# Performance work log

Hardware: AMD Instinct MI355X
Metric: run time of the kernel (lower is better)

## Reference

```python
import jax, jax.numpy as jnp
import numpy as np

D_MODEL = 1024
N_HEAD = 16
D_HEAD = D_MODEL // N_HEAD


def setup_inputs() -> dict:
    key = jax.random.key(0)
    k_x, k_qkv, k_proj = jax.random.split(key, 3)
    B, T = 2, 2048
    x = jax.random.normal(k_x, (B, T, D_MODEL), dtype=jnp.float32)
    # torch Linear weight [out, in]; y = x @ W.T. Scale ~ kaiming-uniform-ish.
    s = 1.0 / np.sqrt(D_MODEL)
    W_qkv = jax.random.uniform(k_qkv, (3 * D_MODEL, D_MODEL), dtype=jnp.float32, minval=-s, maxval=s)
    W_proj = jax.random.uniform(k_proj, (D_MODEL, D_MODEL), dtype=jnp.float32, minval=-s, maxval=s)
    return {"x": x, "W_qkv": W_qkv, "W_proj": W_proj}


def reference(x, W_qkv, W_proj):
    B, T, C = x.shape
    qkv = jnp.einsum('btc,oc->bto', x, W_qkv)  # [B,T,3C]
    q, k, v = jnp.split(qkv, 3, axis=-1)
    # [B,T,C] -> [B,H,T,Dh]
    def heads(t):
        return t.reshape(B, T, N_HEAD, D_HEAD).transpose(0, 2, 1, 3)
    q, k, v = heads(q), heads(k), heads(v)
    scale = 1.0 / np.sqrt(D_HEAD)
    scores = jnp.einsum('bhqd,bhkd->bhqk', q, k) * scale  # [B,H,T,T]
    causal = jnp.tril(jnp.ones((T, T), dtype=bool))
    scores = jnp.where(causal, scores, jnp.finfo(scores.dtype).min)
    attn = jax.nn.softmax(scores, axis=-1)
    y = jnp.einsum('bhqk,bhkd->bhqd', attn, v)  # [B,H,T,Dh]
    y = y.transpose(0, 2, 1, 3).reshape(B, T, C)
    return jnp.einsum('btc,oc->bto', y, W_proj)
```

## Files before the change

kernel.cpp:

```cpp
#include <hip/hip_runtime.h>

typedef unsigned short u16;
typedef float f32x4 __attribute__((ext_vector_type(4)));
typedef __bf16 bf16x8 __attribute__((ext_vector_type(8)));
typedef unsigned int u32x4 __attribute__((ext_vector_type(4)));
typedef u16 u16x4 __attribute__((ext_vector_type(4)));
typedef u16 u16x8 __attribute__((ext_vector_type(8)));

static __device__ __forceinline__ u16 f2bf(float f) {
  union { __bf16 h; u16 u; } c;
  c.h = (__bf16)f;
  return c.u;
}

static __device__ __forceinline__ void gload_lds16(const void* g, void* l) {
  __builtin_amdgcn_global_load_lds(
      (const __attribute__((address_space(1))) unsigned int*)g,
      (__attribute__((address_space(3))) unsigned int*)l, 16, 0, 0);
}

__global__ __launch_bounds__(256) void cvt3_f32_bf16(const float* __restrict__ a,
                                                     const float* __restrict__ bb,
                                                     const float* __restrict__ cc,
                                                     u16* __restrict__ out,
                                                     int n1, int n2, int n3) {
  int i = blockIdx.x * 256 + threadIdx.x;
  const float* src;
  int j = i;
  if (i < n1) { src = a; }
  else if (i < n1 + n2) { src = bb; j = i - n1; }
  else { src = cc; j = i - n1 - n2; if (j >= n3) return; }
  f32x4 v = *((const f32x4*)src + j);
  u16x4 o;
  o[0] = f2bf(v[0]); o[1] = f2bf(v[1]); o[2] = f2bf(v[2]); o[3] = f2bf(v[3]);
  *((u16x4*)out + i) = o;
}

template<int OUT_BF16>
__global__ __launch_bounds__(256) void gemm_nt(const u16* __restrict__ A,
                                               const u16* __restrict__ B,
                                               void* __restrict__ Cp,
                                               int M, int N, int K, int gy) {
  __shared__ __align__(16) u16 lA[128 * 64];
  __shared__ __align__(16) u16 lB[128 * 64];
  const int tid = threadIdx.x;
  const int lane = tid & 63;
  const int wave = tid >> 6;
  const int wm = wave >> 1, wn = wave & 1;
  const int l15 = lane & 15, lg = lane >> 4;

  const int bid = blockIdx.x;
  const int xcd = bid & 7, s = bid >> 3;
  const int pnx = (N >> 7) >> 3;
  const int bm = (s % gy) * 128;
  const int bn = (xcd * pnx + s / gy) * 128;

  f32x4 acc[4][4];
#pragma unroll
  for (int i = 0; i < 4; ++i)
#pragma unroll
    for (int j = 0; j < 4; ++j) acc[i][j] = (f32x4){0.f, 0.f, 0.f, 0.f};

  const u16* Ag[4];
  const u16* Bg[4];
#pragma unroll
  for (int it = 0; it < 4; ++it) {
    const int ss = it * 256 + tid;
    const int row = ss >> 3, g = ss & 7;
    const int gsw = g ^ (row & 7);
    Ag[it] = A + (size_t)(bm + row) * K + gsw * 8;
    Bg[it] = B + (size_t)(bn + row) * K + gsw * 8;
  }

  for (int k0 = 0; k0 < K; k0 += 64) {
#pragma unroll
    for (int it = 0; it < 4; ++it) {
      gload_lds16(Ag[it] + k0, (u16*)lA + (size_t)(it * 256 + tid) * 8);
      gload_lds16(Bg[it] + k0, (u16*)lB + (size_t)(it * 256 + tid) * 8);
    }
    __syncthreads();
#pragma unroll
    for (int kk = 0; kk < 2; ++kk) {
      bf16x8 af[4], bfv[4];
#pragma unroll
      for (int mf = 0; mf < 4; ++mf) {
        const int row = wm * 64 + mf * 16 + l15;
        af[mf] = *(const bf16x8*)((const char*)lA + row * 128 +
                                  ((kk * 64 + lg * 16) ^ ((row & 7) << 4)));
      }
#pragma unroll
      for (int nf = 0; nf < 4; ++nf) {
        const int row = wn * 64 + nf * 16 + l15;
        bfv[nf] = *(const bf16x8*)((const char*)lB + row * 128 +
                                   ((kk * 64 + lg * 16) ^ ((row & 7) << 4)));
      }
#pragma unroll
      for (int mf = 0; mf < 4; ++mf)
#pragma unroll
        for (int nf = 0; nf < 4; ++nf)
          acc[mf][nf] = __builtin_amdgcn_mfma_f32_16x16x32_bf16(af[mf], bfv[nf], acc[mf][nf], 0, 0, 0);
    }
    __syncthreads();
  }

#pragma unroll
  for (int mf = 0; mf < 4; ++mf) {
#pragma unroll
    for (int r = 0; r < 4; ++r) {
      const int row = bm + wm * 64 + mf * 16 + lg * 4 + r;
#pragma unroll
      for (int nf = 0; nf < 4; ++nf) {
        const int col = bn + wn * 64 + nf * 16 + l15;
        const float v = acc[mf][nf][r];
        if (OUT_BF16) ((u16*)Cp)[(size_t)row * N + col] = f2bf(v);
        else          ((float*)Cp)[(size_t)row * N + col] = v;
      }
    }
  }
}

__global__ __launch_bounds__(256) void transpose_v(const u16* __restrict__ qkv,
                                                   u16* __restrict__ vt) {
  constexpr int T = 2048, C3 = 3072, D = 64;
  __shared__ u16 lt[64 * 65];
  const int t0 = blockIdx.x * 64;
  const int bh = blockIdx.y;
  const int b = bh >> 4, h = bh & 15;
  const int tid = threadIdx.x;
#pragma unroll
  for (int it = 0; it < 2; ++it) {
    const int c = tid + it * 256;
    const int tr = c >> 3, d0 = (c & 7) * 8;
    u32x4 v = *(const u32x4*)&qkv[((size_t)b * T + t0 + tr) * C3 + 2048 + h * D + d0];
    const u16* pv = (const u16*)&v;
#pragma unroll
    for (int e = 0; e < 8; ++e) lt[tr * 65 + d0 + e] = pv[e];
  }
  __syncthreads();
#pragma unroll
  for (int it = 0; it < 2; ++it) {
    const int c = tid + it * 256;
    const int d = c >> 3, toff = (c & 7) * 8;
    u16x8 tmp;
#pragma unroll
    for (int e = 0; e < 8; ++e) tmp[e] = lt[(toff + e) * 65 + d];
    *(u16x8*)&vt[((size_t)bh * D + d) * T + t0 + toff] = tmp;
  }
}

__global__ __launch_bounds__(256) void attn_fwd(const u16* __restrict__ qkv,
                                                const u16* __restrict__ vt,
                                                u16* __restrict__ y) {
  constexpr int T = 2048, C = 1024, C3 = 3072, D = 64, NQ = 32;
  __shared__ __align__(16) u16 lK[2][64 * 64];
  __shared__ __align__(16) u16 lV[2][64 * 64];
  __shared__ __align__(16) u16 lP[4 * 16 * 64];
  const int tid = threadIdx.x, lane = tid & 63, w = tid >> 6;
  const int l15 = lane & 15, lg = lane >> 4;

  const int bid = blockIdx.x;
  const int xcd = bid & 7, slot = bid >> 3;
  const int bh = xcd * 4 + (slot >> 4);
  const int pi = slot & 15;
  const int b = bh >> 4, h = bh & 15;

  const int r0 = tid >> 3, off0 = (tid & 7) * 8;
  const int r1 = (tid + 256) >> 3, off1 = off0;
  const int sb0 = (off0 * 2) ^ ((r0 & 7) << 4);
  const int sb1 = (off1 * 2) ^ ((r1 & 7) << 4);
  const u16* Kbase = qkv + (size_t)b * T * C3 + C + h * D;
  const u16* Vbase = vt + (size_t)bh * D * T;

  const float qscale = 0.125f * 1.44269504088896f;

#pragma unroll 1
  for (int qi = 0; qi < 2; ++qi) {
    const int qt = (qi == 0) ? pi : (NQ - 1 - pi);
    const int q0 = qt * 64;

    const size_t qoff = ((size_t)b * T + q0 + w * 16 + l15) * C3 + h * D;
    const bf16x8 aq0 = *(const bf16x8*)&qkv[qoff + lg * 8];
    const bf16x8 aq1 = *(const bf16x8*)&qkv[qoff + 32 + lg * 8];

    float m = -1.0e30f, l = 0.f;
    f32x4 o_acc[4];
#pragma unroll
    for (int nf = 0; nf < 4; ++nf) o_acc[nf] = (f32x4){0.f, 0.f, 0.f, 0.f};

    u32x4 rk0 = *(const u32x4*)(Kbase + (size_t)r0 * C3 + off0);
    u32x4 rk1 = *(const u32x4*)(Kbase + (size_t)r1 * C3 + off1);
    u32x4 rv0 = *(const u32x4*)(Vbase + (size_t)r0 * T + off0);
    u32x4 rv1 = *(const u32x4*)(Vbase + (size_t)r1 * T + off1);
    __syncthreads();
    *(u32x4*)&lK[0][(r0 * 128 + sb0) >> 1] = rk0;
    *(u32x4*)&lK[0][(r1 * 128 + sb1) >> 1] = rk1;
    *(u32x4*)&lV[0][(r0 * 128 + sb0) >> 1] = rv0;
    *(u32x4*)&lV[0][(r1 * 128 + sb1) >> 1] = rv1;
    if (qt > 0) {
      rk0 = *(const u32x4*)(Kbase + (size_t)(64 + r0) * C3 + off0);
      rk1 = *(const u32x4*)(Kbase + (size_t)(64 + r1) * C3 + off1);
      rv0 = *(const u32x4*)(Vbase + (size_t)r0 * T + 64 + off0);
      rv1 = *(const u32x4*)(Vbase + (size_t)r1 * T + 64 + off1);
    }

    for (int kt = 0; kt <= qt; ++kt) {
      const int cur = kt & 1;
      __syncthreads();
      if (kt < qt) {
        *(u32x4*)&lK[cur ^ 1][(r0 * 128 + sb0) >> 1] = rk0;
        *(u32x4*)&lK[cur ^ 1][(r1 * 128 + sb1) >> 1] = rk1;
        *(u32x4*)&lV[cur ^ 1][(r0 * 128 + sb0) >> 1] = rv0;
        *(u32x4*)&lV[cur ^ 1][(r1 * 128 + sb1) >> 1] = rv1;
        if (kt + 1 < qt) {
          const int kn = (kt + 2) * 64;
          rk0 = *(const u32x4*)(Kbase + (size_t)(kn + r0) * C3 + off0);
          rk1 = *(const u32x4*)(Kbase + (size_t)(kn + r1) * C3 + off1);
          rv0 = *(const u32x4*)(Vbase + (size_t)r0 * T + kn + off0);
          rv1 = *(const u32x4*)(Vbase + (size_t)r1 * T + kn + off1);
        }
      }
      const u16* Kc = lK[cur];
      const u16* Vc = lV[cur];

      f32x4 s[4];
#pragma unroll
      for (int nf = 0; nf < 4; ++nf) s[nf] = (f32x4){0.f, 0.f, 0.f, 0.f};
      __builtin_amdgcn_s_setprio(1);
#pragma unroll
      for (int nf = 0; nf < 4; ++nf) {
        const int row = nf * 16 + l15;
        const int x = (row & 7) << 4;
        bf16x8 bk0 = *(const bf16x8*)&Kc[(row * 128 + ((lg * 16) ^ x)) >> 1];
        bf16x8 bk1 = *(const bf16x8*)&Kc[(row * 128 + ((64 + lg * 16) ^ x)) >> 1];
        s[nf] = __builtin_amdgcn_mfma_f32_16x16x32_bf16(bk0, aq0, s[nf], 0, 0, 0);
        s[nf] = __builtin_amdgcn_mfma_f32_16x16x32_bf16(bk1, aq1, s[nf], 0, 0, 0);
      }
      __builtin_amdgcn_s_setprio(0);

#pragma unroll
      for (int nf = 0; nf < 4; ++nf) {
#pragma unroll
        for (int r = 0; r < 4; ++r) {
          float v = s[nf][r] * qscale;
          if (kt == qt) {
            if (nf * 16 + lg * 4 + r > w * 16 + l15) v = -1.0e30f;
          }
          s[nf][r] = v;
        }
      }

      float t0a = fmaxf(fmaxf(s[0][0], s[0][1]), fmaxf(s[0][2], s[0][3]));
      float t1a = fmaxf(fmaxf(s[1][0], s[1][1]), fmaxf(s[1][2], s[1][3]));
      float t2a = fmaxf(fmaxf(s[2][0], s[2][1]), fmaxf(s[2][2], s[2][3]));
      float t3a = fmaxf(fmaxf(s[3][0], s[3][1]), fmaxf(s[3][2], s[3][3]));
      float pmax = fmaxf(fmaxf(t0a, t1a), fmaxf(t2a, t3a));
      pmax = fmaxf(pmax, __shfl_xor(pmax, 16));
      pmax = fmaxf(pmax, __shfl_xor(pmax, 32));

      if (!__all(pmax <= m)) {
        const float mnew = fmaxf(m, pmax);
        const float fct = __builtin_amdgcn_exp2f(m - mnew);
        m = mnew;
        l *= fct;
#pragma unroll
        for (int r = 0; r < 4; ++r) {
          const float fr = __shfl(fct, lg * 4 + r);
#pragma unroll
          for (int nf = 0; nf < 4; ++nf) o_acc[nf][r] *= fr;
        }
      }

      float p[4][4];
#pragma unroll
      for (int nf = 0; nf < 4; ++nf)
#pragma unroll
        for (int r = 0; r < 4; ++r) p[nf][r] = __builtin_amdgcn_exp2f(s[nf][r] - m);
      float s0a = (p[0][0] + p[0][1]) + (p[0][2] + p[0][3]);
      float s1a = (p[1][0] + p[1][1]) + (p[1][2] + p[1][3]);
      float s2a = (p[2][0] + p[2][1]) + (p[2][2] + p[2][3]);
      float s3a = (p[3][0] + p[3][1]) + (p[3][2] + p[3][3]);
      float psum = (s0a + s1a) + (s2a + s3a);
      psum += __shfl_xor(psum, 16);
      psum += __shfl_xor(psum, 32);
      l += psum;

#pragma unroll
      for (int nf = 0; nf < 4; ++nf) {
        u16x4 pk;
        pk[0] = f2bf(p[nf][0]); pk[1] = f2bf(p[nf][1]);
        pk[2] = f2bf(p[nf][2]); pk[3] = f2bf(p[nf][3]);
        *(u16x4*)&lP[(w * 2048 + l15 * 128 + ((nf * 32 + lg * 8) ^ ((l15 & 7) << 4))) >> 1] = pk;
      }

      __builtin_amdgcn_s_setprio(1);
#pragma unroll
      for (int sj = 0; sj < 2; ++sj) {
        bf16x8 ap = *(const bf16x8*)&lP[(w * 2048 + l15 * 128 + ((sj * 64 + lg * 16) ^ ((l15 & 7) << 4))) >> 1];
#pragma unroll
        for (int nf = 0; nf < 4; ++nf) {
          const int d = nf * 16 + l15;
          bf16x8 bv = *(const bf16x8*)&Vc[(d * 128 + ((sj * 64 + lg * 16) ^ ((d & 7) << 4))) >> 1];
          o_acc[nf] = __builtin_amdgcn_mfma_f32_16x16x32_bf16(ap, bv, o_acc[nf], 0, 0, 0);
        }
      }
      __builtin_amdgcn_s_setprio(0);
    }

#pragma unroll
    for (int r = 0; r < 4; ++r) {
      const float li = __builtin_amdgcn_rcpf(__shfl(l, lg * 4 + r));
      const int row = q0 + w * 16 + lg * 4 + r;
#pragma unroll
      for (int nf = 0; nf < 4; ++nf) {
        const int col = h * D + nf * 16 + l15;
        y[((size_t)b * T + row) * C + col] = f2bf(o_acc[nf][r] * li);
      }
    }
  }
}

extern "C" void kernel_launch(void* const* d_in, const int* in_sizes, int n_in,
                              void* d_out, int out_size, void* d_ws, size_t ws_size,
                              hipStream_t stream) {
  const float* x = (const float*)d_in[0];
  const float* Wqkv = (const float*)d_in[1];
  const float* Wproj = (const float*)d_in[2];
  float* out = (float*)d_out;

  constexpr int B = 2, T = 2048, C = 1024, C3 = 3072, H = 16, D = 64;
  constexpr int M = B * T;

  u16* xb = (u16*)d_ws;
  u16* wqkvb = xb + (size_t)M * C;
  u16* wprojb = wqkvb + (size_t)C3 * C;
  u16* qkvb = wprojb + (size_t)C * C;
  u16* vtb = qkvb + (size_t)M * C3;
  u16* yb = vtb + (size_t)M * C;

  constexpr int n1 = (M * C) / 4, n2 = (C3 * C) / 4, n3 = (C * C) / 4;
  cvt3_f32_bf16<<<dim3((n1 + n2 + n3 + 255) / 256), 256, 0, stream>>>(
      x, Wqkv, Wproj, xb, n1, n2, n3);

  gemm_nt<1><<<dim3((C3 / 128) * (M / 128)), 256, 0, stream>>>(xb, wqkvb, qkvb, M, C3, C, M / 128);
  transpose_v<<<dim3(T / 64, B * H), 256, 0, stream>>>(qkvb, vtb);
  attn_fwd<<<dim3(512), 256, 0, stream>>>(qkvb, vtb, yb);
  gemm_nt<0><<<dim3((C / 128) * (M / 128)), 256, 0, stream>>>(yb, wprojb, out, M, C, C, M / 128);
}
```

Before: 115.4 us.

## Fuse V transpose into QKV GEMM epilogue and widen attention key tiles

The QKV GEMM epilogue now writes the V columns directly into the transposed per-head layout, which removes the separate transpose_v kernel launch and its extra read/write pass. The attention kernel also processes 128-key tiles instead of 64, with LDS buffers for K, V and P doubled and the swizzles adjusted. This halves the number of loop iterations and barriers per query tile. The cost is more registers and LDS per block, which may lower occupancy, plus some wasted masked work on the final diagonal tile.

```diff
diff --git a/kernel.cpp b/kernel.cpp
--- a/kernel.cpp
+++ b/kernel.cpp
@@ -36,10 +36,11 @@
   *((u16x4*)out + i) = o;
 }
 
-template<int OUT_BF16>
+template<int OUT_BF16, int FUSE_VT>
 __global__ __launch_bounds__(256) void gemm_nt(const u16* __restrict__ A,
                                                const u16* __restrict__ B,
                                                void* __restrict__ Cp,
+                                               u16* __restrict__ vt,
                                                int M, int N, int K, int gy) {
   __shared__ __align__(16) u16 lA[128 * 64];
   __shared__ __align__(16) u16 lB[128 * 64];
@@ -103,58 +104,46 @@
     __syncthreads();
   }
 
-#pragma unroll
-  for (int mf = 0; mf < 4; ++mf) {
-#pragma unroll
-    for (int r = 0; r < 4; ++r) {
-      const int row = bm + wm * 64 + mf * 16 + lg * 4 + r;
+  if (FUSE_VT && bn >= 2048) {
+#pragma unroll
+    for (int mf = 0; mf < 4; ++mf) {
+      const int row0 = bm + wm * 64 + mf * 16 + lg * 4;
+      const int b = row0 >> 11, t0 = row0 & 2047;
 #pragma unroll
       for (int nf = 0; nf < 4; ++nf) {
-        const int col = bn + wn * 64 + nf * 16 + l15;
-        const float v = acc[mf][nf][r];
-        if (OUT_BF16) ((u16*)Cp)[(size_t)row * N + col] = f2bf(v);
-        else          ((float*)Cp)[(size_t)row * N + col] = v;
-      }
-    }
-  }
-}
-
-__global__ __launch_bounds__(256) void transpose_v(const u16* __restrict__ qkv,
-                                                   u16* __restrict__ vt) {
-  constexpr int T = 2048, C3 = 3072, D = 64;
-  __shared__ u16 lt[64 * 65];
-  const int t0 = blockIdx.x * 64;
-  const int bh = blockIdx.y;
-  const int b = bh >> 4, h = bh & 15;
-  const int tid = threadIdx.x;
-#pragma unroll
-  for (int it = 0; it < 2; ++it) {
-    const int c = tid + it * 256;
-    const int tr = c >> 3, d0 = (c & 7) * 8;
-    u32x4 v = *(const u32x4*)&qkv[((size_t)b * T + t0 + tr) * C3 + 2048 + h * D + d0];
-    const u16* pv = (const u16*)&v;
-#pragma unroll
-    for (int e = 0; e < 8; ++e) lt[tr * 65 + d0 + e] = pv[e];
-  }
-  __syncthreads();
-#pragma unroll
-  for (int it = 0; it < 2; ++it) {
-    const int c = tid + it * 256;
-    const int d = c >> 3, toff = (c & 7) * 8;
-    u16x8 tmp;
-#pragma unroll
-    for (int e = 0; e < 8; ++e) tmp[e] = lt[(toff + e) * 65 + d];
-    *(u16x8*)&vt[((size_t)bh * D + d) * T + t0 + toff] = tmp;
+        const int colv = bn - 2048 + wn * 64 + nf * 16 + l15;
+        const int h = colv >> 6, d = colv & 63;
+        u16x4 pk;
+        pk[0] = f2bf(acc[mf][nf][0]); pk[1] = f2bf(acc[mf][nf][1]);
+        pk[2] = f2bf(acc[mf][nf][2]); pk[3] = f2bf(acc[mf][nf][3]);
+        *(u16x4*)&vt[((size_t)((b * 16 + h) * 64 + d)) * 2048 + t0] = pk;
+      }
+    }
+  } else {
+#pragma unroll
+    for (int mf = 0; mf < 4; ++mf) {
+#pragma unroll
+      for (int r = 0; r < 4; ++r) {
+        const int row = bm + wm * 64 + mf * 16 + lg * 4 + r;
+#pragma unroll
+        for (int nf = 0; nf < 4; ++nf) {
+          const int col = bn + wn * 64 + nf * 16 + l15;
+          const float v = acc[mf][nf][r];
+          if (OUT_BF16) ((u16*)Cp)[(size_t)row * N + col] = f2bf(v);
+          else          ((float*)Cp)[(size_t)row * N + col] = v;
+        }
+      }
+    }
   }
 }
 
 __global__ __launch_bounds__(256) void attn_fwd(const u16* __restrict__ qkv,
                                                 const u16* __restrict__ vt,
                                                 u16* __restrict__ y) {
-  constexpr int T = 2048, C = 1024, C3 = 3072, D = 64, NQ = 32;
-  __shared__ __align__(16) u16 lK[2][64 * 64];
-  __shared__ __align__(16) u16 lV[2][64 * 64];
-  __shared__ __align__(16) u16 lP[4 * 16 * 64];
+  constexpr int T = 2048, C = 1024, C3 = 3072, D = 64, NQ = 32, KB = 128;
+  __shared__ __align__(16) u16 lK[2][KB * 64];
+  __shared__ __align__(16) u16 lV[2][64 * KB];
+  __shared__ __align__(16) u16 lP[4 * 16 * KB];
   const int tid = threadIdx.x, lane = tid & 63, w = tid >> 6;
   const int l15 = lane & 15, lg = lane >> 4;
 
@@ -164,12 +153,18 @@
   const int pi = slot & 15;
   const int b = bh >> 4, h = bh & 15;
 
-  const int r0 = tid >> 3, off0 = (tid & 7) * 8;
-  const int r1 = (tid + 256) >> 3, off1 = off0;
-  const int sb0 = (off0 * 2) ^ ((r0 & 7) << 4);
-  const int sb1 = (off1 * 2) ^ ((r1 & 7) << 4);
+  int kr[4], ko[4], ksb[4], vd[4], vo[4], vsb[4];
+#pragma unroll
+  for (int c = 0; c < 4; ++c) {
+    const int fl = c * 256 + tid;
+    kr[c] = fl >> 3; ko[c] = (fl & 7) * 8;
+    ksb[c] = kr[c] * 128 + ((ko[c] * 2) ^ ((kr[c] & 7) << 4));
+    vd[c] = fl >> 4; vo[c] = (fl & 15) * 8;
+    vsb[c] = vd[c] * 256 + ((vo[c] * 2) ^ ((vd[c] & 15) << 4));
+  }
   const u16* Kbase = qkv + (size_t)b * T * C3 + C + h * D;
   const u16* Vbase = vt + (size_t)bh * D * T;
+  char* lPb = (char*)lP + w * 4096;
 
   const float qscale = 0.125f * 1.44269504088896f;
 
@@ -177,8 +172,10 @@
   for (int qi = 0; qi < 2; ++qi) {
     const int qt = (qi == 0) ? pi : (NQ - 1 - pi);
     const int q0 = qt * 64;
-
-    const size_t qoff = ((size_t)b * T + q0 + w * 16 + l15) * C3 + h * D;
+    const int nkt = (qt + 2) >> 1;
+    const int qrow = q0 + w * 16 + l15;
+
+    const size_t qoff = ((size_t)b * T + qrow) * C3 + h * D;
     const bf16x8 aq0 = *(const bf16x8*)&qkv[qoff + lg * 8];
     const bf16x8 aq1 = *(const bf16x8*)&qkv[qoff + 32 + lg * 8];
 
@@ -187,73 +184,85 @@
 #pragma unroll
     for (int nf = 0; nf < 4; ++nf) o_acc[nf] = (f32x4){0.f, 0.f, 0.f, 0.f};
 
-    u32x4 rk0 = *(const u32x4*)(Kbase + (size_t)r0 * C3 + off0);
-    u32x4 rk1 = *(const u32x4*)(Kbase + (size_t)r1 * C3 + off1);
-    u32x4 rv0 = *(const u32x4*)(Vbase + (size_t)r0 * T + off0);
-    u32x4 rv1 = *(const u32x4*)(Vbase + (size_t)r1 * T + off1);
+    u32x4 rk[4], rv[4];
+#pragma unroll
+    for (int c = 0; c < 4; ++c) {
+      rk[c] = *(const u32x4*)(Kbase + (size_t)kr[c] * C3 + ko[c]);
+      rv[c] = *(const u32x4*)(Vbase + (size_t)vd[c] * T + vo[c]);
+    }
     __syncthreads();
-    *(u32x4*)&lK[0][(r0 * 128 + sb0) >> 1] = rk0;
-    *(u32x4*)&lK[0][(r1 * 128 + sb1) >> 1] = rk1;
-    *(u32x4*)&lV[0][(r0 * 128 + sb0) >> 1] = rv0;
-    *(u32x4*)&lV[0][(r1 * 128 + sb1) >> 1] = rv1;
-    if (qt > 0) {
-      rk0 = *(const u32x4*)(Kbase + (size_t)(64 + r0) * C3 + off0);
-      rk1 = *(const u32x4*)(Kbase + (size_t)(64 + r1) * C3 + off1);
-      rv0 = *(const u32x4*)(Vbase + (size_t)r0 * T + 64 + off0);
-      rv1 = *(const u32x4*)(Vbase + (size_t)r1 * T + 64 + off1);
-    }
-
-    for (int kt = 0; kt <= qt; ++kt) {
+#pragma unroll
+    for (int c = 0; c < 4; ++c) {
+      *(u32x4*)((char*)lK[0] + ksb[c]) = rk[c];
+      *(u32x4*)((char*)lV[0] + vsb[c]) = rv[c];
+    }
+    if (nkt > 1) {
+#pragma unroll
+      for (int c = 0; c < 4; ++c) {
+        rk[c] = *(const u32x4*)(Kbase + (size_t)(KB + kr[c]) * C3 + ko[c]);
+        rv[c] = *(const u32x4*)(Vbase + (size_t)vd[c] * T + KB + vo[c]);
+      }
+    }
+
+    for (int kt = 0; kt < nkt; ++kt) {
       const int cur = kt & 1;
       __syncthreads();
-      if (kt < qt) {
-        *(u32x4*)&lK[cur ^ 1][(r0 * 128 + sb0) >> 1] = rk0;
-        *(u32x4*)&lK[cur ^ 1][(r1 * 128 + sb1) >> 1] = rk1;
-        *(u32x4*)&lV[cur ^ 1][(r0 * 128 + sb0) >> 1] = rv0;
-        *(u32x4*)&lV[cur ^ 1][(r1 * 128 + sb1) >> 1] = rv1;
-        if (kt + 1 < qt) {
-          const int kn = (kt + 2) * 64;
-          rk0 = *(const u32x4*)(Kbase + (size_t)(kn + r0) * C3 + off0);
-          rk1 = *(const u32x4*)(Kbase + (size_t)(kn + r1) * C3 + off1);
-          rv0 = *(const u32x4*)(Vbase + (size_t)r0 * T + kn + off0);
-          rv1 = *(const u32x4*)(Vbase + (size_t)r1 * T + kn + off1);
-        }
-      }
-      const u16* Kc = lK[cur];
-      const u16* Vc = lV[cur];
-
-      f32x4 s[4];
-#pragma unroll
-      for (int nf = 0; nf < 4; ++nf) s[nf] = (f32x4){0.f, 0.f, 0.f, 0.f};
+      if (kt < nkt - 1) {
+#pragma unroll
+        for (int c = 0; c < 4; ++c) {
+          *(u32x4*)((char*)lK[cur ^ 1] + ksb[c]) = rk[c];
+          *(u32x4*)((char*)lV[cur ^ 1] + vsb[c]) = rv[c];
+        }
+        if (kt + 1 < nkt - 1) {
+          const int kn = (kt + 2) * KB;
+#pragma unroll
+          for (int c = 0; c < 4; ++c) {
+            rk[c] = *(const u32x4*)(Kbase + (size_t)(kn + kr[c]) * C3 + ko[c]);
+            rv[c] = *(const u32x4*)(Vbase + (size_t)vd[c] * T + kn + vo[c]);
+          }
+        }
+      }
+      const char* Kc = (const char*)lK[cur];
+      const char* Vc = (const char*)lV[cur];
+
+      f32x4 s[8];
+#pragma unroll
+      for (int nf = 0; nf < 8; ++nf) s[nf] = (f32x4){0.f, 0.f, 0.f, 0.f};
       __builtin_amdgcn_s_setprio(1);
 #pragma unroll
-      for (int nf = 0; nf < 4; ++nf) {
+      for (int nf = 0; nf < 8; ++nf) {
         const int row = nf * 16 + l15;
         const int x = (row & 7) << 4;
-        bf16x8 bk0 = *(const bf16x8*)&Kc[(row * 128 + ((lg * 16) ^ x)) >> 1];
-        bf16x8 bk1 = *(const bf16x8*)&Kc[(row * 128 + ((64 + lg * 16) ^ x)) >> 1];
+        bf16x8 bk0 = *(const bf16x8*)(Kc + row * 128 + ((lg * 16) ^ x));
+        bf16x8 bk1 = *(const bf16x8*)(Kc + row * 128 + ((64 + lg * 16) ^ x));
         s[nf] = __builtin_amdgcn_mfma_f32_16x16x32_bf16(bk0, aq0, s[nf], 0, 0, 0);
         s[nf] = __builtin_amdgcn_mfma_f32_16x16x32_bf16(bk1, aq1, s[nf], 0, 0, 0);
       }
       __builtin_amdgcn_s_setprio(0);
 
-#pragma unroll
-      for (int nf = 0; nf < 4; ++nf) {
-#pragma unroll
-        for (int r = 0; r < 4; ++r) {
-          float v = s[nf][r] * qscale;
-          if (kt == qt) {
-            if (nf * 16 + lg * 4 + r > w * 16 + l15) v = -1.0e30f;
+      if (kt == nkt - 1) {
+        const int qrel = qrow - kt * KB;
+#pragma unroll
+        for (int nf = 0; nf < 8; ++nf)
+#pragma unroll
+          for (int r = 0; r < 4; ++r) {
+            float v = s[nf][r] * qscale;
+            if (nf * 16 + lg * 4 + r > qrel) v = -1.0e30f;
+            s[nf][r] = v;
           }
-          s[nf][r] = v;
-        }
-      }
-
-      float t0a = fmaxf(fmaxf(s[0][0], s[0][1]), fmaxf(s[0][2], s[0][3]));
-      float t1a = fmaxf(fmaxf(s[1][0], s[1][1]), fmaxf(s[1][2], s[1][3]));
-      float t2a = fmaxf(fmaxf(s[2][0], s[2][1]), fmaxf(s[2][2], s[2][3]));
-      float t3a = fmaxf(fmaxf(s[3][0], s[3][1]), fmaxf(s[3][2], s[3][3]));
-      float pmax = fmaxf(fmaxf(t0a, t1a), fmaxf(t2a, t3a));
+      } else {
+#pragma unroll
+        for (int nf = 0; nf < 8; ++nf)
+#pragma unroll
+          for (int r = 0; r < 4; ++r) s[nf][r] *= qscale;
+      }
+
+      float q4[8];
+#pragma unroll
+      for (int nf = 0; nf < 8; ++nf)
+        q4[nf] = fmaxf(fmaxf(s[nf][0], s[nf][1]), fmaxf(s[nf][2], s[nf][3]));
+      float pmax = fmaxf(fmaxf(fmaxf(q4[0], q4[1]), fmaxf(q4[2], q4[3])),
+                         fmaxf(fmaxf(q4[4], q4[5]), fmaxf(q4[6], q4[7])));
       pmax = fmaxf(pmax, __shfl_xor(pmax, 16));
       pmax = fmaxf(pmax, __shfl_xor(pmax, 32));
 
@@ -270,36 +279,35 @@
         }
       }
 
-      float p[4][4];
-#pragma unroll
-      for (int nf = 0; nf < 4; ++nf)
-#pragma unroll
-        for (int r = 0; r < 4; ++r) p[nf][r] = __builtin_amdgcn_exp2f(s[nf][r] - m);
-      float s0a = (p[0][0] + p[0][1]) + (p[0][2] + p[0][3]);
-      float s1a = (p[1][0] + p[1][1]) + (p[1][2] + p[1][3]);
-      float s2a = (p[2][0] + p[2][1]) + (p[2][2] + p[2][3]);
-      float s3a = (p[3][0] + p[3][1]) + (p[3][2] + p[3][3]);
-      float psum = (s0a + s1a) + (s2a + s3a);
+#pragma unroll
+      for (int nf = 0; nf < 8; ++nf)
+#pragma unroll
+        for (int r = 0; r < 4; ++r) s[nf][r] = __builtin_amdgcn_exp2f(s[nf][r] - m);
+      float a4[8];
+#pragma unroll
+      for (int nf = 0; nf < 8; ++nf)
+        a4[nf] = (s[nf][0] + s[nf][1]) + (s[nf][2] + s[nf][3]);
+      float psum = ((a4[0] + a4[1]) + (a4[2] + a4[3])) + ((a4[4] + a4[5]) + (a4[6] + a4[7]));
       psum += __shfl_xor(psum, 16);
       psum += __shfl_xor(psum, 32);
       l += psum;
 
 #pragma unroll
-      for (int nf = 0; nf < 4; ++nf) {
+      for (int nf = 0; nf < 8; ++nf) {
         u16x4 pk;
-        pk[0] = f2bf(p[nf][0]); pk[1] = f2bf(p[nf][1]);
-        pk[2] = f2bf(p[nf][2]); pk[3] = f2bf(p[nf][3]);
-        *(u16x4*)&lP[(w * 2048 + l15 * 128 + ((nf * 32 + lg * 8) ^ ((l15 & 7) << 4))) >> 1] = pk;
+        pk[0] = f2bf(s[nf][0]); pk[1] = f2bf(s[nf][1]);
+        pk[2] = f2bf(s[nf][2]); pk[3] = f2bf(s[nf][3]);
+        *(u16x4*)(lPb + l15 * 256 + ((nf * 32 + lg * 8) ^ (l15 << 4))) = pk;
       }
 
       __builtin_amdgcn_s_setprio(1);
 #pragma unroll
-      for (int sj = 0; sj < 2; ++sj) {
-        bf16x8 ap = *(const bf16x8*)&lP[(w * 2048 + l15 * 128 + ((sj * 64 + lg * 16) ^ ((l15 & 7) << 4))) >> 1];
+      for (int sj = 0; sj < 4; ++sj) {
+        bf16x8 ap = *(const bf16x8*)(lPb + l15 * 256 + ((sj * 64 + lg * 16) ^ (l15 << 4)));
 #pragma unroll
         for (int nf = 0; nf < 4; ++nf) {
           const int d = nf * 16 + l15;
-          bf16x8 bv = *(const bf16x8*)&Vc[(d * 128 + ((sj * 64 + lg * 16) ^ ((d & 7) << 4))) >> 1];
+          bf16x8 bv = *(const bf16x8*)(Vc + d * 256 + ((sj * 64 + lg * 16) ^ ((d & 15) << 4)));
           o_acc[nf] = __builtin_amdgcn_mfma_f32_16x16x32_bf16(ap, bv, o_acc[nf], 0, 0, 0);
         }
       }
@@ -341,8 +349,9 @@
   cvt3_f32_bf16<<<dim3((n1 + n2 + n3 + 255) / 256), 256, 0, stream>>>(
       x, Wqkv, Wproj, xb, n1, n2, n3);
 
-  gemm_nt<1><<<dim3((C3 / 128) * (M / 128)), 256, 0, stream>>>(xb, wqkvb, qkvb, M, C3, C, M / 128);
-  transpose_v<<<dim3(T / 64, B * H), 256, 0, stream>>>(qkvb, vtb);
+  gemm_nt<1, 1><<<dim3((C3 / 128) * (M / 128)), 256, 0, stream>>>(
+      xb, wqkvb, qkvb, vtb, M, C3, C, M / 128);
   attn_fwd<<<dim3(512), 256, 0, stream>>>(qkvb, vtb, yb);
-  gemm_nt<0><<<dim3((C / 128) * (M / 128)), 256, 0, stream>>>(yb, wprojb, out, M, C, C, M / 128);
-}
+  gemm_nt<0, 0><<<dim3((C / 128) * (M / 128)), 256, 0, stream>>>(
+      yb, wprojb, out, nullptr, M, C, C, M / 128);
+}
```

New measurement: 129.4 us. +12.2%, slower.

## Split attention KV range across two blocks and fuse V transpose into QKV GEMM

Applied to the files above, without the earlier changes.

Attention now launches twice as many blocks, each handling half of the causal KV range for a query tile. Each block writes a partial output plus its running max and sum, and a new merge kernel combines the two halves. Separately, the QKV GEMM epilogue writes the V columns directly in transposed layout, which removes the standalone transpose kernel. The aim is more parallelism and better occupancy in attention and one fewer launch, at the cost of an extra merge kernel, partial-output round trips through memory, and a second bf16 rounding of the partial outputs.

```diff
diff --git a/kernel.cpp b/kernel.cpp
--- a/kernel.cpp
+++ b/kernel.cpp
@@ -11,6 +11,11 @@
   union { __bf16 h; u16 u; } c;
   c.h = (__bf16)f;
   return c.u;
+}
+static __device__ __forceinline__ float bf2f(u16 u) {
+  union { unsigned u; float f; } c;
+  c.u = ((unsigned)u) << 16;
+  return c.f;
 }
 
 static __device__ __forceinline__ void gload_lds16(const void* g, void* l) {
@@ -36,10 +41,11 @@
   *((u16x4*)out + i) = o;
 }
 
-template<int OUT_BF16>
+template<int OUT_BF16, int FUSE_VT>
 __global__ __launch_bounds__(256) void gemm_nt(const u16* __restrict__ A,
                                                const u16* __restrict__ B,
                                                void* __restrict__ Cp,
+                                               u16* __restrict__ vt,
                                                int M, int N, int K, int gy) {
   __shared__ __align__(16) u16 lA[128 * 64];
   __shared__ __align__(16) u16 lB[128 * 64];
@@ -103,54 +109,43 @@
     __syncthreads();
   }
 
-#pragma unroll
-  for (int mf = 0; mf < 4; ++mf) {
-#pragma unroll
-    for (int r = 0; r < 4; ++r) {
-      const int row = bm + wm * 64 + mf * 16 + lg * 4 + r;
+  if (FUSE_VT && bn >= 2048) {
+#pragma unroll
+    for (int mf = 0; mf < 4; ++mf) {
+      const int row0 = bm + wm * 64 + mf * 16 + lg * 4;
+      const int b = row0 >> 11, t0 = row0 & 2047;
 #pragma unroll
       for (int nf = 0; nf < 4; ++nf) {
-        const int col = bn + wn * 64 + nf * 16 + l15;
-        const float v = acc[mf][nf][r];
-        if (OUT_BF16) ((u16*)Cp)[(size_t)row * N + col] = f2bf(v);
-        else          ((float*)Cp)[(size_t)row * N + col] = v;
-      }
-    }
-  }
-}
-
-__global__ __launch_bounds__(256) void transpose_v(const u16* __restrict__ qkv,
-                                                   u16* __restrict__ vt) {
-  constexpr int T = 2048, C3 = 3072, D = 64;
-  __shared__ u16 lt[64 * 65];
-  const int t0 = blockIdx.x * 64;
-  const int bh = blockIdx.y;
-  const int b = bh >> 4, h = bh & 15;
-  const int tid = threadIdx.x;
-#pragma unroll
-  for (int it = 0; it < 2; ++it) {
-    const int c = tid + it * 256;
-    const int tr = c >> 3, d0 = (c & 7) * 8;
-    u32x4 v = *(const u32x4*)&qkv[((size_t)b * T + t0 + tr) * C3 + 2048 + h * D + d0];
-    const u16* pv = (const u16*)&v;
-#pragma unroll
-    for (int e = 0; e < 8; ++e) lt[tr * 65 + d0 + e] = pv[e];
-  }
-  __syncthreads();
-#pragma unroll
-  for (int it = 0; it < 2; ++it) {
-    const int c = tid + it * 256;
-    const int d = c >> 3, toff = (c & 7) * 8;
-    u16x8 tmp;
-#pragma unroll
-    for (int e = 0; e < 8; ++e) tmp[e] = lt[(toff + e) * 65 + d];
-    *(u16x8*)&vt[((size_t)bh * D + d) * T + t0 + toff] = tmp;
+        const int colv = bn - 2048 + wn * 64 + nf * 16 + l15;
+        const int h = colv >> 6, d = colv & 63;
+        u16x4 pk;
+        pk[0] = f2bf(acc[mf][nf][0]); pk[1] = f2bf(acc[mf][nf][1]);
+        pk[2] = f2bf(acc[mf][nf][2]); pk[3] = f2bf(acc[mf][nf][3]);
+        *(u16x4*)&vt[((size_t)((b * 16 + h) * 64 + d)) * 2048 + t0] = pk;
+      }
+    }
+  } else {
+#pragma unroll
+    for (int mf = 0; mf < 4; ++mf) {
+#pragma unroll
+      for (int r = 0; r < 4; ++r) {
+        const int row = bm + wm * 64 + mf * 16 + lg * 4 + r;
+#pragma unroll
+        for (int nf = 0; nf < 4; ++nf) {
+          const int col = bn + wn * 64 + nf * 16 + l15;
+          const float v = acc[mf][nf][r];
+          if (OUT_BF16) ((u16*)Cp)[(size_t)row * N + col] = f2bf(v);
+          else          ((float*)Cp)[(size_t)row * N + col] = v;
+        }
+      }
+    }
   }
 }
 
 __global__ __launch_bounds__(256) void attn_fwd(const u16* __restrict__ qkv,
                                                 const u16* __restrict__ vt,
-                                                u16* __restrict__ y) {
+                                                u16* __restrict__ po,
+                                                float* __restrict__ mlf) {
   constexpr int T = 2048, C = 1024, C3 = 3072, D = 64, NQ = 32;
   __shared__ __align__(16) u16 lK[2][64 * 64];
   __shared__ __align__(16) u16 lV[2][64 * 64];
@@ -159,15 +154,16 @@
   const int l15 = lane & 15, lg = lane >> 4;
 
   const int bid = blockIdx.x;
-  const int xcd = bid & 7, slot = bid >> 3;
-  const int bh = xcd * 4 + (slot >> 4);
-  const int pi = slot & 15;
+  const int xcd = bid & 7, rest = bid >> 3;
+  const int bhl = rest >> 5, r5 = rest & 31;
+  const int pi = r5 >> 1, hf = r5 & 1;
+  const int bh = xcd * 4 + bhl;
   const int b = bh >> 4, h = bh & 15;
 
   const int r0 = tid >> 3, off0 = (tid & 7) * 8;
-  const int r1 = (tid + 256) >> 3, off1 = off0;
+  const int r1 = (tid + 256) >> 3;
   const int sb0 = (off0 * 2) ^ ((r0 & 7) << 4);
-  const int sb1 = (off1 * 2) ^ ((r1 & 7) << 4);
+  const int sb1 = (off0 * 2) ^ ((r1 & 7) << 4);
   const u16* Kbase = qkv + (size_t)b * T * C3 + C + h * D;
   const u16* Vbase = vt + (size_t)bh * D * T;
 
@@ -177,6 +173,10 @@
   for (int qi = 0; qi < 2; ++qi) {
     const int qt = (qi == 0) ? pi : (NQ - 1 - pi);
     const int q0 = qt * 64;
+    const int h0 = (qt + 2) >> 1;
+    const int kts = hf ? h0 : 0;
+    const int kte = hf ? (qt + 1) : h0;
+    const int nit = kte - kts;
 
     const size_t qoff = ((size_t)b * T + q0 + w * 16 + l15) * C3 + h * D;
     const bf16x8 aq0 = *(const bf16x8*)&qkv[qoff + lg * 8];
@@ -187,136 +187,171 @@
 #pragma unroll
     for (int nf = 0; nf < 4; ++nf) o_acc[nf] = (f32x4){0.f, 0.f, 0.f, 0.f};
 
-    u32x4 rk0 = *(const u32x4*)(Kbase + (size_t)r0 * C3 + off0);
-    u32x4 rk1 = *(const u32x4*)(Kbase + (size_t)r1 * C3 + off1);
-    u32x4 rv0 = *(const u32x4*)(Vbase + (size_t)r0 * T + off0);
-    u32x4 rv1 = *(const u32x4*)(Vbase + (size_t)r1 * T + off1);
-    __syncthreads();
-    *(u32x4*)&lK[0][(r0 * 128 + sb0) >> 1] = rk0;
-    *(u32x4*)&lK[0][(r1 * 128 + sb1) >> 1] = rk1;
-    *(u32x4*)&lV[0][(r0 * 128 + sb0) >> 1] = rv0;
-    *(u32x4*)&lV[0][(r1 * 128 + sb1) >> 1] = rv1;
-    if (qt > 0) {
-      rk0 = *(const u32x4*)(Kbase + (size_t)(64 + r0) * C3 + off0);
-      rk1 = *(const u32x4*)(Kbase + (size_t)(64 + r1) * C3 + off1);
-      rv0 = *(const u32x4*)(Vbase + (size_t)r0 * T + 64 + off0);
-      rv1 = *(const u32x4*)(Vbase + (size_t)r1 * T + 64 + off1);
-    }
-
-    for (int kt = 0; kt <= qt; ++kt) {
-      const int cur = kt & 1;
+    if (nit > 0) {
+      const int kb0 = kts * 64;
+      u32x4 rk0 = *(const u32x4*)(Kbase + (size_t)(kb0 + r0) * C3 + off0);
+      u32x4 rk1 = *(const u32x4*)(Kbase + (size_t)(kb0 + r1) * C3 + off0);
+      u32x4 rv0 = *(const u32x4*)(Vbase + (size_t)r0 * T + kb0 + off0);
+      u32x4 rv1 = *(const u32x4*)(Vbase + (size_t)r1 * T + kb0 + off0);
       __syncthreads();
-      if (kt < qt) {
-        *(u32x4*)&lK[cur ^ 1][(r0 * 128 + sb0) >> 1] = rk0;
-        *(u32x4*)&lK[cur ^ 1][(r1 * 128 + sb1) >> 1] = rk1;
-        *(u32x4*)&lV[cur ^ 1][(r0 * 128 + sb0) >> 1] = rv0;
-        *(u32x4*)&lV[cur ^ 1][(r1 * 128 + sb1) >> 1] = rv1;
-        if (kt + 1 < qt) {
-          const int kn = (kt + 2) * 64;
-          rk0 = *(const u32x4*)(Kbase + (size_t)(kn + r0) * C3 + off0);
-          rk1 = *(const u32x4*)(Kbase + (size_t)(kn + r1) * C3 + off1);
-          rv0 = *(const u32x4*)(Vbase + (size_t)r0 * T + kn + off0);
-          rv1 = *(const u32x4*)(Vbase + (size_t)r1 * T + kn + off1);
-        }
-      }
-      const u16* Kc = lK[cur];
-      const u16* Vc = lV[cur];
-
-      f32x4 s[4];
-#pragma unroll
-      for (int nf = 0; nf < 4; ++nf) s[nf] = (f32x4){0.f, 0.f, 0.f, 0.f};
-      __builtin_amdgcn_s_setprio(1);
-#pragma unroll
-      for (int nf = 0; nf < 4; ++nf) {
-        const int row = nf * 16 + l15;
-        const int x = (row & 7) << 4;
-        bf16x8 bk0 = *(const bf16x8*)&Kc[(row * 128 + ((lg * 16) ^ x)) >> 1];
-        bf16x8 bk1 = *(const bf16x8*)&Kc[(row * 128 + ((64 + lg * 16) ^ x)) >> 1];
-        s[nf] = __builtin_amdgcn_mfma_f32_16x16x32_bf16(bk0, aq0, s[nf], 0, 0, 0);
-        s[nf] = __builtin_amdgcn_mfma_f32_16x16x32_bf16(bk1, aq1, s[nf], 0, 0, 0);
-      }
-      __builtin_amdgcn_s_setprio(0);
-
-#pragma unroll
-      for (int nf = 0; nf < 4; ++nf) {
-#pragma unroll
-        for (int r = 0; r < 4; ++r) {
-          float v = s[nf][r] * qscale;
-          if (kt == qt) {
-            if (nf * 16 + lg * 4 + r > w * 16 + l15) v = -1.0e30f;
+      *(u32x4*)&lK[0][(r0 * 128 + sb0) >> 1] = rk0;
+      *(u32x4*)&lK[0][(r1 * 128 + sb1) >> 1] = rk1;
+      *(u32x4*)&lV[0][(r0 * 128 + sb0) >> 1] = rv0;
+      *(u32x4*)&lV[0][(r1 * 128 + sb1) >> 1] = rv1;
+      if (nit > 1) {
+        const int kb1 = kb0 + 64;
+        rk0 = *(const u32x4*)(Kbase + (size_t)(kb1 + r0) * C3 + off0);
+        rk1 = *(const u32x4*)(Kbase + (size_t)(kb1 + r1) * C3 + off0);
+        rv0 = *(const u32x4*)(Vbase + (size_t)r0 * T + kb1 + off0);
+        rv1 = *(const u32x4*)(Vbase + (size_t)r1 * T + kb1 + off0);
+      }
+
+      for (int i = 0; i < nit; ++i) {
+        const int kt = kts + i;
+        const int cur = i & 1;
+        __syncthreads();
+        if (i < nit - 1) {
+          *(u32x4*)&lK[cur ^ 1][(r0 * 128 + sb0) >> 1] = rk0;
+          *(u32x4*)&lK[cur ^ 1][(r1 * 128 + sb1) >> 1] = rk1;
+          *(u32x4*)&lV[cur ^ 1][(r0 * 128 + sb0) >> 1] = rv0;
+          *(u32x4*)&lV[cur ^ 1][(r1 * 128 + sb1) >> 1] = rv1;
+          if (i + 1 < nit - 1) {
+            const int kn = (kt + 2) * 64;
+            rk0 = *(const u32x4*)(Kbase + (size_t)(kn + r0) * C3 + off0);
+            rk1 = *(const u32x4*)(Kbase + (size_t)(kn + r1) * C3 + off0);
+            rv0 = *(const u32x4*)(Vbase + (size_t)r0 * T + kn + off0);
+            rv1 = *(const u32x4*)(Vbase + (size_t)r1 * T + kn + off0);
           }
-          s[nf][r] = v;
-        }
-      }
-
-      float t0a = fmaxf(fmaxf(s[0][0], s[0][1]), fmaxf(s[0][2], s[0][3]));
-      float t1a = fmaxf(fmaxf(s[1][0], s[1][1]), fmaxf(s[1][2], s[1][3]));
-      float t2a = fmaxf(fmaxf(s[2][0], s[2][1]), fmaxf(s[2][2], s[2][3]));
-      float t3a = fmaxf(fmaxf(s[3][0], s[3][1]), fmaxf(s[3][2], s[3][3]));
-      float pmax = fmaxf(fmaxf(t0a, t1a), fmaxf(t2a, t3a));
-      pmax = fmaxf(pmax, __shfl_xor(pmax, 16));
-      pmax = fmaxf(pmax, __shfl_xor(pmax, 32));
-
-      if (!__all(pmax <= m)) {
-        const float mnew = fmaxf(m, pmax);
-        const float fct = __builtin_amdgcn_exp2f(m - mnew);
-        m = mnew;
-        l *= fct;
-#pragma unroll
-        for (int r = 0; r < 4; ++r) {
-          const float fr = __shfl(fct, lg * 4 + r);
-#pragma unroll
-          for (int nf = 0; nf < 4; ++nf) o_acc[nf][r] *= fr;
-        }
-      }
-
-      float p[4][4];
-#pragma unroll
-      for (int nf = 0; nf < 4; ++nf)
-#pragma unroll
-        for (int r = 0; r < 4; ++r) p[nf][r] = __builtin_amdgcn_exp2f(s[nf][r] - m);
-      float s0a = (p[0][0] + p[0][1]) + (p[0][2] + p[0][3]);
-      float s1a = (p[1][0] + p[1][1]) + (p[1][2] + p[1][3]);
-      float s2a = (p[2][0] + p[2][1]) + (p[2][2] + p[2][3]);
-      float s3a = (p[3][0] + p[3][1]) + (p[3][2] + p[3][3]);
-      float psum = (s0a + s1a) + (s2a + s3a);
-      psum += __shfl_xor(psum, 16);
-      psum += __shfl_xor(psum, 32);
-      l += psum;
-
-#pragma unroll
-      for (int nf = 0; nf < 4; ++nf) {
-        u16x4 pk;
-        pk[0] = f2bf(p[nf][0]); pk[1] = f2bf(p[nf][1]);
-        pk[2] = f2bf(p[nf][2]); pk[3] = f2bf(p[nf][3]);
-        *(u16x4*)&lP[(w * 2048 + l15 * 128 + ((nf * 32 + lg * 8) ^ ((l15 & 7) << 4))) >> 1] = pk;
-      }
-
-      __builtin_amdgcn_s_setprio(1);
-#pragma unroll
-      for (int sj = 0; sj < 2; ++sj) {
-        bf16x8 ap = *(const bf16x8*)&lP[(w * 2048 + l15 * 128 + ((sj * 64 + lg * 16) ^ ((l15 & 7) << 4))) >> 1];
+        }
+        const u16* Kc = lK[cur];
+        const u16* Vc = lV[cur];
+
+        f32x4 s[4];
+#pragma unroll
+        for (int nf = 0; nf < 4; ++nf) s[nf] = (f32x4){0.f, 0.f, 0.f, 0.f};
+        __builtin_amdgcn_s_setprio(1);
 #pragma unroll
         for (int nf = 0; nf < 4; ++nf) {
-          const int d = nf * 16 + l15;
-          bf16x8 bv = *(const bf16x8*)&Vc[(d * 128 + ((sj * 64 + lg * 16) ^ ((d & 7) << 4))) >> 1];
-          o_acc[nf] = __builtin_amdgcn_mfma_f32_16x16x32_bf16(ap, bv, o_acc[nf], 0, 0, 0);
-        }
-      }
-      __builtin_amdgcn_s_setprio(0);
-    }
-
+          const int row = nf * 16 + l15;
+          const int x = (row & 7) << 4;
+          bf16x8 bk0 = *(const bf16x8*)&Kc[(row * 128 + ((lg * 16) ^ x)) >> 1];
+          bf16x8 bk1 = *(const bf16x8*)&Kc[(row * 128 + ((64 + lg * 16) ^ x)) >> 1];
+          s[nf] = __builtin_amdgcn_mfma_f32_16x16x32_bf16(bk0, aq0, s[nf], 0, 0, 0);
+          s[nf] = __builtin_amdgcn_mfma_f32_16x16x32_bf16(bk1, aq1, s[nf], 0, 0, 0);
+        }
+        __builtin_amdgcn_s_setprio(0);
+
+#pragma unroll
+        for (int nf = 0; nf < 4; ++nf) {
+#pragma unroll
+          for (int r = 0; r < 4; ++r) {
+            float v = s[nf][r] * qscale;
+            if (kt == qt) {
+              if (nf * 16 + lg * 4 + r > w * 16 + l15) v = -1.0e30f;
+            }
+            s[nf][r] = v;
+          }
+        }
+
+        float t0a = fmaxf(fmaxf(s[0][0], s[0][1]), fmaxf(s[0][2], s[0][3]));
+        float t1a = fmaxf(fmaxf(s[1][0], s[1][1]), fmaxf(s[1][2], s[1][3]));
+        float t2a = fmaxf(fmaxf(s[2][0], s[2][1]), fmaxf(s[2][2], s[2][3]));
+        float t3a = fmaxf(fmaxf(s[3][0], s[3][1]), fmaxf(s[3][2], s[3][3]));
+        float pmax = fmaxf(fmaxf(t0a, t1a), fmaxf(t2a, t3a));
+        pmax = fmaxf(pmax, __shfl_xor(pmax, 16));
+        pmax = fmaxf(pmax, __shfl_xor(pmax, 32));
+
+        if (!__all(pmax <= m)) {
+          const float mnew = fmaxf(m, pmax);
+          const float fct = __builtin_amdgcn_exp2f(m - mnew);
+          m = mnew;
+          l *= fct;
+#pragma unroll
+          for (int r = 0; r < 4; ++r) {
+            const float fr = __shfl(fct, lg * 4 + r);
+#pragma unroll
+            for (int nf = 0; nf < 4; ++nf) o_acc[nf][r] *= fr;
+          }
+        }
+
+        float p[4][4];
+#pragma unroll
+        for (int nf = 0; nf < 4; ++nf)
+#pragma unroll
+          for (int r = 0; r < 4; ++r) p[nf][r] = __builtin_amdgcn_exp2f(s[nf][r] - m);
+        float s0a = (p[0][0] + p[0][1]) + (p[0][2] + p[0][3]);
+        float s1a = (p[1][0] + p[1][1]) + (p[1][2] + p[1][3]);
+        float s2a = (p[2][0] + p[2][1]) + (p[2][2] + p[2][3]);
+        float s3a = (p[3][0] + p[3][1]) + (p[3][2] + p[3][3]);
+        float psum = (s0a + s1a) + (s2a + s3a);
+        psum += __shfl_xor(psum, 16);
+        psum += __shfl_xor(psum, 32);
+        l += psum;
+
+#pragma unroll
+        for (int nf = 0; nf < 4; ++nf) {
+          u16x4 pk;
+          pk[0] = f2bf(p[nf][0]); pk[1] = f2bf(p[nf][1]);
+          pk[2] = f2bf(p[nf][2]); pk[3] = f2bf(p[nf][3]);
+          *(u16x4*)&lP[(w * 2048 + l15 * 128 + ((nf * 32 + lg * 8) ^ ((l15 & 7) << 4))) >> 1] = pk;
+        }
+
+        __builtin_amdgcn_s_setprio(1);
+#pragma unroll
+        for (int sj = 0; sj < 2; ++sj) {
+          bf16x8 ap = *(const bf16x8*)&lP[(w * 2048 + l15 * 128 + ((sj * 64 + lg * 16) ^ ((l15 & 7) << 4))) >> 1];
+#pragma unroll
+          for (int nf = 0; nf < 4; ++nf) {
+            const int d = nf * 16 + l15;
+            bf16x8 bv = *(const bf16x8*)&Vc[(d * 128 + ((sj * 64 + lg * 16) ^ ((d & 7) << 4))) >> 1];
+            o_acc[nf] = __builtin_amdgcn_mfma_f32_16x16x32_bf16(ap, bv, o_acc[nf], 0, 0, 0);
+          }
+        }
+        __builtin_amdgcn_s_setprio(0);
+      }
+    }
+
+    u16* pob = po + (size_t)hf * (4096ull * 1024ull);
 #pragma unroll
     for (int r = 0; r < 4; ++r) {
-      const float li = __builtin_amdgcn_rcpf(__shfl(l, lg * 4 + r));
+      const float lv = __shfl(l, lg * 4 + r);
+      const float li = (lv > 0.f) ? __builtin_amdgcn_rcpf(lv) : 0.f;
       const int row = q0 + w * 16 + lg * 4 + r;
 #pragma unroll
       for (int nf = 0; nf < 4; ++nf) {
         const int col = h * D + nf * 16 + l15;
-        y[((size_t)b * T + row) * C + col] = f2bf(o_acc[nf][r] * li);
-      }
+        pob[((size_t)b * T + row) * C + col] = f2bf(o_acc[nf][r] * li);
+      }
+    }
+    if (lg == 0) {
+      const size_t idx = (size_t)(b * T + q0 + w * 16 + l15) * 16 + h;
+      float* mp = mlf + (size_t)hf * 131072ull + idx * 2;
+      mp[0] = m;
+      mp[1] = l;
     }
   }
+}
+
+__global__ __launch_bounds__(256) void merge_o(const u16* __restrict__ po,
+                                               const float* __restrict__ mlf,
+                                               u16* __restrict__ y) {
+  const int gid = blockIdx.x * 256 + threadIdx.x;
+  const int row = gid >> 3, d0 = (gid & 7) * 8;
+  const int bt = row >> 4, h = row & 15;
+  const float m1 = mlf[row * 2], l1 = mlf[row * 2 + 1];
+  const float m2 = mlf[131072 + row * 2], l2 = mlf[131072 + row * 2 + 1];
+  const float ms = fmaxf(m1, m2);
+  const float a1 = l1 * __builtin_amdgcn_exp2f(m1 - ms);
+  const float a2 = l2 * __builtin_amdgcn_exp2f(m2 - ms);
+  const float inv = __builtin_amdgcn_rcpf(a1 + a2);
+  const float w1 = a1 * inv, w2 = a2 * inv;
+  const size_t off = (size_t)bt * 1024 + h * 64 + d0;
+  u16x8 p1 = *(const u16x8*)&po[off];
+  u16x8 p2 = *(const u16x8*)&po[4194304ull + off];
+  u16x8 o;
+#pragma unroll
+  for (int j = 0; j < 8; ++j) o[j] = f2bf(w1 * bf2f(p1[j]) + w2 * bf2f(p2[j]));
+  *(u16x8*)&y[off] = o;
 }
 
 extern "C" void kernel_launch(void* const* d_in, const int* in_sizes, int n_in,
@@ -336,13 +371,17 @@
   u16* qkvb = wprojb + (size_t)C * C;
   u16* vtb = qkvb + (size_t)M * C3;
   u16* yb = vtb + (size_t)M * C;
+  u16* po = yb + (size_t)M * C;
+  float* mlf = (float*)(po + 2ull * M * C);
 
   constexpr int n1 = (M * C) / 4, n2 = (C3 * C) / 4, n3 = (C * C) / 4;
   cvt3_f32_bf16<<<dim3((n1 + n2 + n3 + 255) / 256), 256, 0, stream>>>(
       x, Wqkv, Wproj, xb, n1, n2, n3);
 
-  gemm_nt<1><<<dim3((C3 / 128) * (M / 128)), 256, 0, stream>>>(xb, wqkvb, qkvb, M, C3, C, M / 128);
-  transpose_v<<<dim3(T / 64, B * H), 256, 0, stream>>>(qkvb, vtb);
-  attn_fwd<<<dim3(512), 256, 0, stream>>>(qkvb, vtb, yb);
-  gemm_nt<0><<<dim3((C / 128) * (M / 128)), 256, 0, stream>>>(yb, wprojb, out, M, C, C, M / 128);
-}
+  gemm_nt<1, 1><<<dim3((C3 / 128) * (M / 128)), 256, 0, stream>>>(
+      xb, wqkvb, qkvb, vtb, M, C3, C, M / 128);
+  attn_fwd<<<dim3(1024), 256, 0, stream>>>(qkvb, vtb, po, mlf);
+  merge_o<<<dim3(2048), 256, 0, stream>>>(po, mlf, yb);
+  gemm_nt<0, 0><<<dim3((C / 128) * (M / 128)), 256, 0, stream>>>(
+      yb, wprojb, out, nullptr, M, C, C, M / 128);
+}
```

After: 123.5 us. +7.1%, slower.
